# Kernel optimization log

Hardware: AMD Instinct MI355X
Metric: run time of the kernel (lower is better)

The kernel has to match this reference:

```python
import jax, jax.numpy as jnp
import numpy as np

N_HEAD = 16
N_FEAT = 1024
HEAD_DIM = N_FEAT // N_HEAD


def setup_inputs() -> dict:
    key = jax.random.key(0)
    ks = jax.random.split(key, 13)
    B, Tq, Tc = 2, 1024, 1024
    s = 0.02
    return {
        "query": jax.random.normal(ks[0], (B, Tq, N_FEAT), jnp.float32),
        "key": jax.random.normal(ks[1], (B, Tq, N_FEAT), jnp.float32),
        "value": jax.random.normal(ks[2], (B, Tq, N_FEAT), jnp.float32),
        "cache": jax.random.normal(ks[3], (B, N_HEAD, Tc, 2 * HEAD_DIM), jnp.float32),
        "Wq": jax.random.normal(ks[4], (N_FEAT, N_FEAT), jnp.float32) * s,
        "bq": jax.random.normal(ks[5], (N_FEAT,), jnp.float32) * s,
        "Wk": jax.random.normal(ks[6], (N_FEAT, N_FEAT), jnp.float32) * s,
        "bk": jax.random.normal(ks[7], (N_FEAT,), jnp.float32) * s,
        "Wv": jax.random.normal(ks[8], (N_FEAT, N_FEAT), jnp.float32) * s,
        "bv": jax.random.normal(ks[9], (N_FEAT,), jnp.float32) * s,
        "Wo": jax.random.normal(ks[10], (N_FEAT, N_FEAT), jnp.float32) * s,
        "bo": jax.random.normal(ks[11], (N_FEAT,), jnp.float32) * s,
    }


def _split_heads(x, B):
    # [B, T, C] -> [B, H, T, D]
    return x.reshape(B, -1, N_HEAD, HEAD_DIM).transpose(0, 2, 1, 3)


def reference(query, key, value, cache, Wq, bq, Wk, bk, Wv, bv, Wo, bo):
    B, Tq, _ = query.shape
    # torch Linear: y = x @ W.T + b
    q = _split_heads(query @ Wq.T + bq, B)   # [B,H,Tq,D]
    k = _split_heads(key @ Wk.T + bk, B)     # [B,H,Tk,D]
    v = _split_heads(value @ Wv.T + bv, B)
    # KV-cache concat (cache holds [K | V] along last dim)
    k_cache, v_cache = jnp.split(cache, 2, axis=-1)
    k = jnp.concatenate([k_cache, k], axis=2)
    v = jnp.concatenate([v_cache, v], axis=2)
    new_cache = jnp.concatenate([k, v], axis=-1)
    scores = jnp.einsum("bhqd,bhkd->bhqk", q, k) / np.sqrt(HEAD_DIM).astype(jnp.float32)
    attn = jax.nn.softmax(scores, axis=-1)  # fake mask path; dropout is identity (rate 0 / eval)
    x = jnp.einsum("bhqk,bhkd->bhqd", attn, v)
    x = x.transpose(0, 2, 1, 3).reshape(B, Tq, N_FEAT)
    out = x @ Wo.T + bo
    return out, new_cache
```

## Files before the change

### kernel.cpp

```cpp
#include <hip/hip_runtime.h>

typedef short short4s __attribute__((ext_vector_type(4)));
typedef short short8 __attribute__((ext_vector_type(8)));
typedef __bf16 bf16x8 __attribute__((ext_vector_type(8)));
typedef float f32x4 __attribute__((ext_vector_type(4)));

#define NFEAT 1024
#define HDIM  64
#define NHEAD 16
#define TC2   2048
#define QSCL  0.18033688011112043f

__device__ __forceinline__ short f2bf(float f) {
    unsigned int u = __builtin_bit_cast(unsigned int, f);
    u += 0x7fffu + ((u >> 16) & 1u);
    return (short)(u >> 16);
}
__device__ __forceinline__ short f2bfq(float f) {
    __bf16 h = (__bf16)f;
    return __builtin_bit_cast(short, h);
}
__device__ __forceinline__ float bf2f(short s) {
    unsigned int u = ((unsigned int)(unsigned short)s) << 16;
    return __builtin_bit_cast(float, u);
}

__device__ __forceinline__ f32x4 mfma_bf16(short8 a, short8 b, f32x4 c) {
    return __builtin_amdgcn_mfma_f32_16x16x32_bf16(
        __builtin_bit_cast(bf16x8, a), __builtin_bit_cast(bf16x8, b), c, 0, 0, 0);
}

#define GLOAD16(gp, lp) __builtin_amdgcn_global_load_lds( \
    (const __attribute__((address_space(1))) void*)(gp),  \
    (__attribute__((address_space(3))) void*)(lp), 16, 0, 0)

__global__ __launch_bounds__(256) void prep_kernel(
    const float* __restrict__ q, const float* __restrict__ k, const float* __restrict__ v,
    const float* __restrict__ Wq, const float* __restrict__ Wk,
    const float* __restrict__ Wv, const float* __restrict__ Wo,
    const float4* __restrict__ cache4,
    short* __restrict__ qin, short* __restrict__ kin, short* __restrict__ vin,
    short* __restrict__ wqb, short* __restrict__ wkb, short* __restrict__ wvb,
    short* __restrict__ wob,
    float4* __restrict__ nc4, short* __restrict__ kbb, short* __restrict__ vtb)
{
    const int b = blockIdx.x, tid = threadIdx.x;
    if (b < 5120) {
        const float* src; short* dst; size_t base;
        if (b < 1024)      { src = q;  dst = qin; base = (size_t)b * 2048; }
        else if (b < 2048) { src = k;  dst = kin; base = (size_t)(b - 1024) * 2048; }
        else if (b < 3072) { src = v;  dst = vin; base = (size_t)(b - 2048) * 2048; }
        else if (b < 3584) { src = Wq; dst = wqb; base = (size_t)(b - 3072) * 2048; }
        else if (b < 4096) { src = Wk; dst = wkb; base = (size_t)(b - 3584) * 2048; }
        else if (b < 4608) { src = Wv; dst = wvb; base = (size_t)(b - 4096) * 2048; }
        else               { src = Wo; dst = wob; base = (size_t)(b - 4608) * 2048; }
        size_t i = base + (size_t)tid * 8;
        float4 a0 = *(const float4*)(src + i);
        float4 a1 = *(const float4*)(src + i + 4);
        short8 o;
        o[0] = f2bf(a0.x); o[1] = f2bf(a0.y); o[2] = f2bf(a0.z); o[3] = f2bf(a0.w);
        o[4] = f2bf(a1.x); o[5] = f2bf(a1.y); o[6] = f2bf(a1.z); o[7] = f2bf(a1.w);
        *(short8*)(dst + i) = o;
    } else {
        int i = (b - 5120) * 256 + tid;
        int c4 = i & 31;
        int t  = (i >> 5) & 1023;
        int bh = i >> 15;
        float4 val = cache4[i];
        nc4[((size_t)bh * TC2 + t) * 32 + c4] = val;
        int c = c4 * 4;
        if (c < 64) {
            size_t base = ((size_t)bh * TC2 + t) * HDIM + c;
            kbb[base + 0] = f2bf(val.x); kbb[base + 1] = f2bf(val.y);
            kbb[base + 2] = f2bf(val.z); kbb[base + 3] = f2bf(val.w);
        } else {
            int d = c - 64;
            size_t base = ((size_t)bh * HDIM + d) * TC2 + t;
            vtb[base + 0 * TC2] = f2bf(val.x); vtb[base + 1 * TC2] = f2bf(val.y);
            vtb[base + 2 * TC2] = f2bf(val.z); vtb[base + 3 * TC2] = f2bf(val.w);
        }
    }
}

__global__ __launch_bounds__(256) void gemm128(
    const short* __restrict__ A0, const short* __restrict__ A1, const short* __restrict__ A2,
    const short* __restrict__ W0, const short* __restrict__ W1, const short* __restrict__ W2,
    const float* __restrict__ b0, const float* __restrict__ b1, const float* __restrict__ b2,
    float* __restrict__ outf, short* __restrict__ qbuf,
    short* __restrict__ kbb, short* __restrict__ vtb, int base_mode)
{
    __shared__ short As[128 * 64];
    __shared__ short Bs[128 * 64];

    int mode;
    const short *A, *W;
    const float* bias;
    if (base_mode == 3) { mode = 3; A = A0; W = W0; bias = b0; }
    else {
        mode = blockIdx.z;
        if (mode == 0)      { A = A0; W = W0; bias = b0; }
        else if (mode == 1) { A = A1; W = W1; bias = b1; }
        else                { A = A2; W = W2; bias = b2; }
    }

    const int tid = threadIdx.x, lane = tid & 63, w = tid >> 6;
    const int wr = w >> 1, wc = w & 1;
    const int lr = lane & 15, lg = lane >> 4;
    const int bx = blockIdx.x, by = blockIdx.y;

    f32x4 acc[4][4];
#pragma unroll
    for (int m = 0; m < 4; ++m)
#pragma unroll
        for (int n = 0; n < 4; ++n) acc[m][n] = (f32x4){0.f, 0.f, 0.f, 0.f};

    const short* agBase = A + (size_t)(by * 128 + w * 32 + (lane >> 3)) * 1024 + (lane & 7) * 8;
    const short* bgBase = W + (size_t)(bx * 128 + w * 32 + (lane >> 3)) * 1024 + (lane & 7) * 8;
    short* asW = &As[w * 2048];
    short* bsW = &Bs[w * 2048];

    for (int kt = 0; kt < 16; ++kt) {
        const short* ag = agBase + kt * 64;
        const short* bg = bgBase + kt * 64;
        GLOAD16(ag,          asW);
        GLOAD16(ag + 8192,   asW + 512);
        GLOAD16(ag + 16384,  asW + 1024);
        GLOAD16(ag + 24576,  asW + 1536);
        GLOAD16(bg,          bsW);
        GLOAD16(bg + 8192,   bsW + 512);
        GLOAD16(bg + 16384,  bsW + 1024);
        GLOAD16(bg + 24576,  bsW + 1536);
        __syncthreads();
#pragma unroll
        for (int kk = 0; kk < 2; ++kk) {
            short8 af[4], bf[4];
#pragma unroll
            for (int m = 0; m < 4; ++m)
                af[m] = *(const short8*)&As[(wr * 64 + m * 16 + lr) * 64 + kk * 32 + lg * 8];
#pragma unroll
            for (int n = 0; n < 4; ++n)
                bf[n] = *(const short8*)&Bs[(wc * 64 + n * 16 + lr) * 64 + kk * 32 + lg * 8];
#pragma unroll
            for (int m = 0; m < 4; ++m)
#pragma unroll
                for (int n = 0; n < 4; ++n)
                    acc[m][n] = mfma_bf16(af[m], bf[n], acc[m][n]);
        }
        __syncthreads();
    }

#pragma unroll
    for (int m = 0; m < 4; ++m) {
#pragma unroll
        for (int n = 0; n < 4; ++n) {
            const int cg = bx * 128 + wc * 64 + n * 16 + lr;
            const int rg0 = by * 128 + wr * 64 + m * 16 + lg * 4;
            const float bv = bias[cg];
            if (mode == 3) {
#pragma unroll
                for (int r = 0; r < 4; ++r)
                    outf[(size_t)(rg0 + r) * NFEAT + cg] = acc[m][n][r] + bv;
            } else {
                const int b = rg0 >> 10, t0 = rg0 & 1023;
                const int h = cg >> 6, d = cg & 63;
                const size_t bh = (size_t)b * NHEAD + h;
                if (mode == 0) {
#pragma unroll
                    for (int r = 0; r < 4; ++r)
                        qbuf[(bh * 1024 + t0 + r) * HDIM + d] = f2bf((acc[m][n][r] + bv) * QSCL);
                } else if (mode == 1) {
#pragma unroll
                    for (int r = 0; r < 4; ++r) {
                        float val = acc[m][n][r] + bv;
                        outf[(bh * TC2 + 1024 + t0 + r) * 128 + d] = val;
                        kbb[(bh * TC2 + 1024 + t0 + r) * HDIM + d] = f2bf(val);
                    }
                } else {
                    short4s pk;
#pragma unroll
                    for (int r = 0; r < 4; ++r) {
                        float val = acc[m][n][r] + bv;
                        outf[(bh * TC2 + 1024 + t0 + r) * 128 + 64 + d] = val;
                        pk[r] = f2bf(val);
                    }
                    *(short4s*)&vtb[(bh * HDIM + d) * TC2 + 1024 + t0] = pk;
                }
            }
        }
    }
}

__global__ __launch_bounds__(512) void attn_kernel(
    const short* __restrict__ qb, const short* __restrict__ kb,
    const short* __restrict__ vtb, short* __restrict__ opart, float* __restrict__ mlbuf)
{
    __shared__ short Ks[2][64 * 64];
    __shared__ short Vs[2][64 * 64];
    __shared__ short Ps[8][16 * 64];

    const int tid = threadIdx.x, lane = tid & 63, w = tid >> 6;
    const int lr = lane & 15, lg = lane >> 4;
    const int b0 = blockIdx.x;
    const int xcd = b0 & 7, rest = b0 >> 3;
    const int unit = xcd + 8 * (rest & 15);
    const int qt = rest >> 4;
    const int bh = unit >> 2, quarter = unit & 3;
    const int xz = lr & 7;

    const short* qrow = qb + ((size_t)bh * 1024 + qt * 128 + w * 16 + lr) * HDIM + lg * 8;
    const short8 bq0 = *(const short8*)(qrow);
    const short8 bq1 = *(const short8*)(qrow + 32);

    const int srow = tid >> 3;
    const int scx = ((tid & 7) ^ (srow & 7)) * 8;
    const short* kgb = kb  + ((size_t)bh * TC2 + quarter * 512 + srow) * HDIM + scx;
    const short* vgb = vtb + ((size_t)bh * HDIM + srow) * TC2 + quarter * 512 + scx;
    short* kdst = &Ks[0][0] + w * 512;
    short* vdst = &Vs[0][0] + w * 512;

#define STAGE(bufsel, kvt_) do {                                         \
        const short* kg_ = kgb + (size_t)(kvt_) * 64 * HDIM;             \
        const short* vg_ = vgb + (kvt_) * 64;                            \
        GLOAD16(kg_, kdst + (bufsel) * 4096);                            \
        GLOAD16(vg_, vdst + (bufsel) * 4096);                            \
    } while (0)

    f32x4 accx[4];
#pragma unroll
    for (int i = 0; i < 4; ++i) accx[i] = (f32x4){0.f, 0.f, 0.f, 0.f};
    float ms = -3.0e38f, ls = 0.f;
    short* pw = &Ps[w][0];

    STAGE(0, 0);
    __syncthreads();

    int cur = 0;
    for (int kvt = 0; kvt < 8; ++kvt) {
        if (kvt < 7) STAGE(cur ^ 1, kvt + 1);
        const short* Kc = &Ks[cur][0];
        const short* Vc = &Vs[cur][0];

        f32x4 s[4];
#pragma unroll
        for (int n = 0; n < 4; ++n) {
            const short* kt = Kc + (n * 16 + lr) * 64;
            short8 k0 = *(const short8*)&kt[(lg ^ xz) * 8];
            short8 k1 = *(const short8*)&kt[((4 + lg) ^ xz) * 8];
            s[n] = (f32x4){0.f, 0.f, 0.f, 0.f};
            s[n] = mfma_bf16(k0, bq0, s[n]);
            s[n] = mfma_bf16(k1, bq1, s[n]);
        }

        float v8[8];
#pragma unroll
        for (int i = 0; i < 8; ++i) v8[i] = fmaxf(s[i >> 1][(i & 1) * 2], s[i >> 1][(i & 1) * 2 + 1]);
        float v4a = fmaxf(v8[0], v8[1]), v4b = fmaxf(v8[2], v8[3]);
        float v4c = fmaxf(v8[4], v8[5]), v4d = fmaxf(v8[6], v8[7]);
        float pmax = fmaxf(fmaxf(v4a, v4b), fmaxf(v4c, v4d));
        pmax = fmaxf(pmax, __shfl_xor(pmax, 16));
        pmax = fmaxf(pmax, __shfl_xor(pmax, 32));

        if (!__all(pmax - ms <= 8.0f)) {
            float mn = fmaxf(ms, pmax);
            float alpha = __builtin_amdgcn_exp2f(ms - mn);
            ms = mn;
            ls *= alpha;
            float ar[4];
#pragma unroll
            for (int r = 0; r < 4; ++r) ar[r] = __shfl(alpha, lg * 4 + r);
#pragma unroll
            for (int nd = 0; nd < 4; ++nd)
#pragma unroll
                for (int r = 0; r < 4; ++r) accx[nd][r] *= ar[r];
        }

        float p[4][4];
        float sm[8];
#pragma unroll
        for (int n = 0; n < 4; ++n)
#pragma unroll
            for (int r = 0; r < 4; ++r) p[n][r] = __builtin_amdgcn_exp2f(s[n][r] - ms);
#pragma unroll
        for (int i = 0; i < 8; ++i) sm[i] = p[i >> 1][(i & 1) * 2] + p[i >> 1][(i & 1) * 2 + 1];
        float rs = ((sm[0] + sm[1]) + (sm[2] + sm[3])) + ((sm[4] + sm[5]) + (sm[6] + sm[7]));
        rs += __shfl_xor(rs, 16);
        rs += __shfl_xor(rs, 32);
        ls += rs;

#pragma unroll
        for (int n = 0; n < 4; ++n) {
            short4s pk;
            pk[0] = f2bfq(p[n][0]); pk[1] = f2bfq(p[n][1]);
            pk[2] = f2bfq(p[n][2]); pk[3] = f2bfq(p[n][3]);
            int slot = (2 * n + (lg >> 1)) ^ xz;
            *(short4s*)&pw[lr * 64 + slot * 8 + (lg & 1) * 4] = pk;
        }

        short8 ap0 = *(const short8*)&pw[lr * 64 + (lg ^ xz) * 8];
        short8 ap1 = *(const short8*)&pw[lr * 64 + ((4 + lg) ^ xz) * 8];
#pragma unroll
        for (int nd = 0; nd < 4; ++nd) {
            const short* vt = Vc + (nd * 16 + lr) * 64;
            short8 vf0 = *(const short8*)&vt[(lg ^ xz) * 8];
            short8 vf1 = *(const short8*)&vt[((4 + lg) ^ xz) * 8];
            accx[nd] = mfma_bf16(ap0, vf0, accx[nd]);
            accx[nd] = mfma_bf16(ap1, vf1, accx[nd]);
        }

        __syncthreads();
        cur ^= 1;
    }

    const size_t rbase = (size_t)quarter * 32768 + (size_t)bh * 1024 + qt * 128 + w * 16;
#pragma unroll
    for (int nd = 0; nd < 4; ++nd)
#pragma unroll
        for (int r = 0; r < 4; ++r)
            opart[(rbase + lg * 4 + r) * 64 + nd * 16 + lr] = f2bfq(accx[nd][r]);
    if (lg == 0) {
        mlbuf[(rbase + lr) * 2]     = ms;
        mlbuf[(rbase + lr) * 2 + 1] = ls;
    }
#undef STAGE
}

__global__ __launch_bounds__(256) void combine_kernel(
    const short* __restrict__ opart, const float* __restrict__ mlbuf,
    short* __restrict__ xb)
{
    int idx = blockIdx.x * 256 + threadIdx.x;
    int r = idx >> 3, d8 = (idx & 7) * 8;
    float m[4], l[4];
#pragma unroll
    for (int i = 0; i < 4; ++i) {
        m[i] = mlbuf[((size_t)i * 32768 + r) * 2];
        l[i] = mlbuf[((size_t)i * 32768 + r) * 2 + 1];
    }
    float M = fmaxf(fmaxf(m[0], m[1]), fmaxf(m[2], m[3]));
    float acc[8];
#pragma unroll
    for (int j = 0; j < 8; ++j) acc[j] = 0.f;
    float lsum = 0.f;
#pragma unroll
    for (int i = 0; i < 4; ++i) {
        float wi = __builtin_amdgcn_exp2f(m[i] - M);
        lsum += l[i] * wi;
        short8 op = *(const short8*)&opart[((size_t)i * 32768 + r) * 64 + d8];
#pragma unroll
        for (int j = 0; j < 8; ++j) acc[j] += bf2f(op[j]) * wi;
    }
    float inv = 1.0f / lsum;
    short8 o;
#pragma unroll
    for (int j = 0; j < 8; ++j) o[j] = f2bfq(acc[j] * inv);
    int bh = r >> 10, tq = r & 1023;
    int b = bh >> 4, h = bh & 15;
    *(short8*)&xb[((size_t)(b * 1024 + tq)) * NFEAT + h * 64 + d8] = o;
}

extern "C" void kernel_launch(void* const* d_in, const int* in_sizes, int n_in,
                              void* d_out, int out_size, void* d_ws, size_t ws_size,
                              hipStream_t stream) {
    const float* query = (const float*)d_in[0];
    const float* key   = (const float*)d_in[1];
    const float* value = (const float*)d_in[2];
    const float* cache = (const float*)d_in[3];
    const float* Wq = (const float*)d_in[4];
    const float* bq = (const float*)d_in[5];
    const float* Wk = (const float*)d_in[6];
    const float* bk = (const float*)d_in[7];
    const float* Wv = (const float*)d_in[8];
    const float* bv = (const float*)d_in[9];
    const float* Wo = (const float*)d_in[10];
    const float* bo = (const float*)d_in[11];

    float* out0   = (float*)d_out;
    float* ncache = out0 + (size_t)2 * 1024 * 1024;

    short* qin = (short*)d_ws;
    short* kin = qin + (size_t)2097152;
    short* vin = kin + (size_t)2097152;
    short* wqb = vin + (size_t)2097152;
    short* wkb = wqb + (size_t)1048576;
    short* wvb = wkb + (size_t)1048576;
    short* wob = wvb + (size_t)1048576;
    short* qbuf = wob + (size_t)1048576;
    short* kbb  = qbuf + (size_t)2097152;
    short* vtb  = kbb  + (size_t)4194304;
    short* opart = (short*)d_ws;
    float* mlbuf = (float*)(qin + (size_t)8388608);
    short* xb    = qbuf;

    prep_kernel<<<9216, 256, 0, stream>>>(query, key, value, Wq, Wk, Wv, Wo,
        (const float4*)cache, qin, kin, vin, wqb, wkb, wvb, wob,
        (float4*)ncache, kbb, vtb);

    gemm128<<<dim3(8, 16, 3), 256, 0, stream>>>(qin, kin, vin, wqb, wkb, wvb,
        bq, bk, bv, ncache, qbuf, kbb, vtb, 0);

    attn_kernel<<<1024, 512, 0, stream>>>(qbuf, kbb, vtb, opart, mlbuf);

    combine_kernel<<<1024, 256, 0, stream>>>(opart, mlbuf, xb);

    gemm128<<<dim3(8, 16, 1), 256, 0, stream>>>(xb, nullptr, nullptr, wob, nullptr, nullptr,
        bo, nullptr, nullptr, out0, nullptr, nullptr, nullptr, 3);
}
```

Measured before the change: 117.2 us.

## Shrink GEMM tiles, LDS-transpose V cache, split V transpose kernel, halve P staging

The GEMMs move from 128x128 to 64x128 tiles, doubling the grid to fill more CUs. The prep kernel's per-element scattered V transpose writes are replaced with an LDS-staged transpose that issues coalesced 16-byte stores. The transposed V for the projection is now built by a separate vtrans kernel that reads the fp32 new cache, rather than by strided writes in the GEMM epilogue. The attention kernel stages P in two half-width chunks with sched barriers, which cuts its LDS footprint. The costs are an extra launch, an extra read of fp32 V, and less operand reuse per GEMM tile.

```diff
diff --git a/kernel.cpp b/kernel.cpp
--- a/kernel.cpp
+++ b/kernel.cpp
@@ -44,6 +44,7 @@
     short* __restrict__ wob,
     float4* __restrict__ nc4, short* __restrict__ kbb, short* __restrict__ vtb)
 {
+    __shared__ short Vt[64 * 72];
     const int b = blockIdx.x, tid = threadIdx.x;
     if (b < 5120) {
         const float* src; short* dst; size_t base;
@@ -62,34 +63,75 @@
         o[4] = f2bf(a1.x); o[5] = f2bf(a1.y); o[6] = f2bf(a1.z); o[7] = f2bf(a1.w);
         *(short8*)(dst + i) = o;
     } else {
-        int i = (b - 5120) * 256 + tid;
-        int c4 = i & 31;
-        int t  = (i >> 5) & 1023;
-        int bh = i >> 15;
-        float4 val = cache4[i];
-        nc4[((size_t)bh * TC2 + t) * 32 + c4] = val;
-        int c = c4 * 4;
-        if (c < 64) {
-            size_t base = ((size_t)bh * TC2 + t) * HDIM + c;
-            kbb[base + 0] = f2bf(val.x); kbb[base + 1] = f2bf(val.y);
-            kbb[base + 2] = f2bf(val.z); kbb[base + 3] = f2bf(val.w);
+        const int cb = b - 5120;
+        const int bh = cb >> 4, t0 = (cb & 15) * 64;
+        const int r = tid >> 2, qb4 = (tid & 3) * 8;
+        const float4* src = cache4 + ((size_t)bh * 1024 + t0 + r) * 32 + qb4;
+        float4* ncr = nc4 + ((size_t)bh * TC2 + t0 + r) * 32 + qb4;
+        if (qb4 < 16) {
+            short* kd = &kbb[((size_t)bh * TC2 + t0 + r) * 64 + qb4 * 4];
+#pragma unroll
+            for (int j = 0; j < 8; ++j) {
+                float4 val = src[j];
+                ncr[j] = val;
+                short4s kp;
+                kp[0] = f2bf(val.x); kp[1] = f2bf(val.y);
+                kp[2] = f2bf(val.z); kp[3] = f2bf(val.w);
+                *(short4s*)(kd + j * 4) = kp;
+            }
         } else {
-            int d = c - 64;
-            size_t base = ((size_t)bh * HDIM + d) * TC2 + t;
-            vtb[base + 0 * TC2] = f2bf(val.x); vtb[base + 1 * TC2] = f2bf(val.y);
-            vtb[base + 2 * TC2] = f2bf(val.z); vtb[base + 3 * TC2] = f2bf(val.w);
-        }
-    }
-}
-
-__global__ __launch_bounds__(256) void gemm128(
+#pragma unroll
+            for (int j = 0; j < 8; ++j) {
+                float4 val = src[j];
+                ncr[j] = val;
+                int d = qb4 * 4 - 64 + j * 4;
+                Vt[(d + 0) * 72 + r] = f2bf(val.x);
+                Vt[(d + 1) * 72 + r] = f2bf(val.y);
+                Vt[(d + 2) * 72 + r] = f2bf(val.z);
+                Vt[(d + 3) * 72 + r] = f2bf(val.w);
+            }
+        }
+        __syncthreads();
+        const int d = tid >> 2, seg = (tid & 3) * 16;
+        short* vd = &vtb[((size_t)bh * HDIM + d) * TC2 + t0 + seg];
+        *(short8*)(vd)     = *(const short8*)&Vt[d * 72 + seg];
+        *(short8*)(vd + 8) = *(const short8*)&Vt[d * 72 + seg + 8];
+    }
+}
+
+__global__ __launch_bounds__(256) void vtrans_kernel(
+    const float* __restrict__ nc, short* __restrict__ vtb)
+{
+    __shared__ short Vt[64 * 72];
+    const int cb = blockIdx.x;
+    const int bh = cb >> 4, t0 = 1024 + (cb & 15) * 64;
+    const int tid = threadIdx.x;
+    const int r = tid >> 2, dseg = (tid & 3) * 16;
+    const float4* src = (const float4*)(nc + ((size_t)bh * TC2 + t0 + r) * 128 + 64 + dseg);
+#pragma unroll
+    for (int j = 0; j < 4; ++j) {
+        float4 val = src[j];
+        int d = dseg + j * 4;
+        Vt[(d + 0) * 72 + r] = f2bf(val.x);
+        Vt[(d + 1) * 72 + r] = f2bf(val.y);
+        Vt[(d + 2) * 72 + r] = f2bf(val.z);
+        Vt[(d + 3) * 72 + r] = f2bf(val.w);
+    }
+    __syncthreads();
+    const int d = tid >> 2, seg = (tid & 3) * 16;
+    short* vd = &vtb[((size_t)bh * HDIM + d) * TC2 + t0 + seg];
+    *(short8*)(vd)     = *(const short8*)&Vt[d * 72 + seg];
+    *(short8*)(vd + 8) = *(const short8*)&Vt[d * 72 + seg + 8];
+}
+
+__global__ __launch_bounds__(256) void gemm64(
     const short* __restrict__ A0, const short* __restrict__ A1, const short* __restrict__ A2,
     const short* __restrict__ W0, const short* __restrict__ W1, const short* __restrict__ W2,
     const float* __restrict__ b0, const float* __restrict__ b1, const float* __restrict__ b2,
-    float* __restrict__ outf, short* __restrict__ qbuf,
-    short* __restrict__ kbb, short* __restrict__ vtb, int base_mode)
+    float* __restrict__ outf, short* __restrict__ qbuf, short* __restrict__ kbb,
+    int base_mode)
 {
-    __shared__ short As[128 * 64];
+    __shared__ short As[64 * 64];
     __shared__ short Bs[128 * 64];
 
     int mode;
@@ -104,19 +146,18 @@
     }
 
     const int tid = threadIdx.x, lane = tid & 63, w = tid >> 6;
-    const int wr = w >> 1, wc = w & 1;
     const int lr = lane & 15, lg = lane >> 4;
     const int bx = blockIdx.x, by = blockIdx.y;
 
-    f32x4 acc[4][4];
+    f32x4 acc[4][2];
 #pragma unroll
     for (int m = 0; m < 4; ++m)
 #pragma unroll
-        for (int n = 0; n < 4; ++n) acc[m][n] = (f32x4){0.f, 0.f, 0.f, 0.f};
-
-    const short* agBase = A + (size_t)(by * 128 + w * 32 + (lane >> 3)) * 1024 + (lane & 7) * 8;
+        for (int n = 0; n < 2; ++n) acc[m][n] = (f32x4){0.f, 0.f, 0.f, 0.f};
+
+    const short* agBase = A + (size_t)(by * 64 + w * 16 + (lane >> 3)) * 1024 + (lane & 7) * 8;
     const short* bgBase = W + (size_t)(bx * 128 + w * 32 + (lane >> 3)) * 1024 + (lane & 7) * 8;
-    short* asW = &As[w * 2048];
+    short* asW = &As[w * 1024];
     short* bsW = &Bs[w * 2048];
 
     for (int kt = 0; kt < 16; ++kt) {
@@ -124,8 +165,6 @@
         const short* bg = bgBase + kt * 64;
         GLOAD16(ag,          asW);
         GLOAD16(ag + 8192,   asW + 512);
-        GLOAD16(ag + 16384,  asW + 1024);
-        GLOAD16(ag + 24576,  asW + 1536);
         GLOAD16(bg,          bsW);
         GLOAD16(bg + 8192,   bsW + 512);
         GLOAD16(bg + 16384,  bsW + 1024);
@@ -133,17 +172,17 @@
         __syncthreads();
 #pragma unroll
         for (int kk = 0; kk < 2; ++kk) {
-            short8 af[4], bf[4];
+            short8 af[4], bf[2];
 #pragma unroll
             for (int m = 0; m < 4; ++m)
-                af[m] = *(const short8*)&As[(wr * 64 + m * 16 + lr) * 64 + kk * 32 + lg * 8];
-#pragma unroll
-            for (int n = 0; n < 4; ++n)
-                bf[n] = *(const short8*)&Bs[(wc * 64 + n * 16 + lr) * 64 + kk * 32 + lg * 8];
+                af[m] = *(const short8*)&As[(m * 16 + lr) * 64 + kk * 32 + lg * 8];
+#pragma unroll
+            for (int n = 0; n < 2; ++n)
+                bf[n] = *(const short8*)&Bs[(w * 32 + n * 16 + lr) * 64 + kk * 32 + lg * 8];
 #pragma unroll
             for (int m = 0; m < 4; ++m)
 #pragma unroll
-                for (int n = 0; n < 4; ++n)
+                for (int n = 0; n < 2; ++n)
                     acc[m][n] = mfma_bf16(af[m], bf[n], acc[m][n]);
         }
         __syncthreads();
@@ -152,9 +191,9 @@
 #pragma unroll
     for (int m = 0; m < 4; ++m) {
 #pragma unroll
-        for (int n = 0; n < 4; ++n) {
-            const int cg = bx * 128 + wc * 64 + n * 16 + lr;
-            const int rg0 = by * 128 + wr * 64 + m * 16 + lg * 4;
+        for (int n = 0; n < 2; ++n) {
+            const int cg = bx * 128 + w * 32 + n * 16 + lr;
+            const int rg0 = by * 64 + m * 16 + lg * 4;
             const float bv = bias[cg];
             if (mode == 3) {
 #pragma unroll
@@ -176,14 +215,9 @@
                         kbb[(bh * TC2 + 1024 + t0 + r) * HDIM + d] = f2bf(val);
                     }
                 } else {
-                    short4s pk;
-#pragma unroll
-                    for (int r = 0; r < 4; ++r) {
-                        float val = acc[m][n][r] + bv;
-                        outf[(bh * TC2 + 1024 + t0 + r) * 128 + 64 + d] = val;
-                        pk[r] = f2bf(val);
-                    }
-                    *(short4s*)&vtb[(bh * HDIM + d) * TC2 + 1024 + t0] = pk;
+#pragma unroll
+                    for (int r = 0; r < 4; ++r)
+                        outf[(bh * TC2 + 1024 + t0 + r) * 128 + 64 + d] = acc[m][n][r] + bv;
                 }
             }
         }
@@ -196,7 +230,7 @@
 {
     __shared__ short Ks[2][64 * 64];
     __shared__ short Vs[2][64 * 64];
-    __shared__ short Ps[8][16 * 64];
+    __shared__ short Ps[8][16 * 32];
 
     const int tid = threadIdx.x, lane = tid & 63, w = tid >> 6;
     const int lr = lane & 15, lg = lane >> 4;
@@ -288,23 +322,24 @@
         ls += rs;
 
 #pragma unroll
-        for (int n = 0; n < 4; ++n) {
-            short4s pk;
-            pk[0] = f2bfq(p[n][0]); pk[1] = f2bfq(p[n][1]);
-            pk[2] = f2bfq(p[n][2]); pk[3] = f2bfq(p[n][3]);
-            int slot = (2 * n + (lg >> 1)) ^ xz;
-            *(short4s*)&pw[lr * 64 + slot * 8 + (lg & 1) * 4] = pk;
-        }
-
-        short8 ap0 = *(const short8*)&pw[lr * 64 + (lg ^ xz) * 8];
-        short8 ap1 = *(const short8*)&pw[lr * 64 + ((4 + lg) ^ xz) * 8];
-#pragma unroll
-        for (int nd = 0; nd < 4; ++nd) {
-            const short* vt = Vc + (nd * 16 + lr) * 64;
-            short8 vf0 = *(const short8*)&vt[(lg ^ xz) * 8];
-            short8 vf1 = *(const short8*)&vt[((4 + lg) ^ xz) * 8];
-            accx[nd] = mfma_bf16(ap0, vf0, accx[nd]);
-            accx[nd] = mfma_bf16(ap1, vf1, accx[nd]);
+        for (int ks = 0; ks < 2; ++ks) {
+            __builtin_amdgcn_sched_barrier(0);
+#pragma unroll
+            for (int np = 0; np < 2; ++np) {
+                int n = 2 * ks + np;
+                short4s pk;
+                pk[0] = f2bfq(p[n][0]); pk[1] = f2bfq(p[n][1]);
+                pk[2] = f2bfq(p[n][2]); pk[3] = f2bfq(p[n][3]);
+                int slot = (2 * np + (lg >> 1)) ^ (lr & 3);
+                *(short4s*)&pw[lr * 32 + slot * 8 + (lg & 1) * 4] = pk;
+            }
+            short8 ap = *(const short8*)&pw[lr * 32 + (lg ^ (lr & 3)) * 8];
+#pragma unroll
+            for (int nd = 0; nd < 4; ++nd) {
+                const short* vt = Vc + (nd * 16 + lr) * 64;
+                short8 vf = *(const short8*)&vt[((ks * 4 + lg) ^ xz) * 8];
+                accx[nd] = mfma_bf16(ap, vf, accx[nd]);
+            }
         }
 
         __syncthreads();
@@ -391,17 +426,19 @@
     float* mlbuf = (float*)(qin + (size_t)8388608);
     short* xb    = qbuf;
 
-    prep_kernel<<<9216, 256, 0, stream>>>(query, key, value, Wq, Wk, Wv, Wo,
+    prep_kernel<<<5632, 256, 0, stream>>>(query, key, value, Wq, Wk, Wv, Wo,
         (const float4*)cache, qin, kin, vin, wqb, wkb, wvb, wob,
         (float4*)ncache, kbb, vtb);
 
-    gemm128<<<dim3(8, 16, 3), 256, 0, stream>>>(qin, kin, vin, wqb, wkb, wvb,
-        bq, bk, bv, ncache, qbuf, kbb, vtb, 0);
+    gemm64<<<dim3(8, 32, 3), 256, 0, stream>>>(qin, kin, vin, wqb, wkb, wvb,
+        bq, bk, bv, ncache, qbuf, kbb, 0);
+
+    vtrans_kernel<<<512, 256, 0, stream>>>(ncache, vtb);
 
     attn_kernel<<<1024, 512, 0, stream>>>(qbuf, kbb, vtb, opart, mlbuf);
 
     combine_kernel<<<1024, 256, 0, stream>>>(opart, mlbuf, xb);
 
-    gemm128<<<dim3(8, 16, 1), 256, 0, stream>>>(xb, nullptr, nullptr, wob, nullptr, nullptr,
-        bo, nullptr, nullptr, out0, nullptr, nullptr, nullptr, 3);
-}
+    gemm64<<<dim3(8, 32, 1), 256, 0, stream>>>(xb, nullptr, nullptr, wob, nullptr, nullptr,
+        bo, nullptr, nullptr, out0, nullptr, nullptr, 3);
+}
```

Result: slower. 122.5 us (+4.5%).
